# Optimization experiments

Hardware: AMD Instinct MI355X
Metric: run time of the kernel (lower is better)

Reference implementation:

```python
import jax, jax.numpy as jnp
import numpy as np

H, NH, NKV, HD, FF = 2048, 16, 8, 128, 6144
S, T = 2048, 4096
EPS, THETA, NEG = 1e-6, 1e6, -1e9

def _rms(x, w, eps=EPS):
    return x * jax.lax.rsqrt(jnp.mean(x * x, axis=-1, keepdims=True) + eps) * w

def _rotate_half(x):
    d = x.shape[-1] // 2
    return jnp.concatenate([-x[..., d:], x[..., :d]], axis=-1)

def _rope(positions, hd, theta=THETA):
    inv_freq = 1.0 / (theta ** (jnp.arange(0, hd, 2, dtype=jnp.float32) / hd))
    freqs = positions.astype(jnp.float32)[..., None] * inv_freq  # [B,S,hd/2]
    emb = jnp.concatenate([freqs, freqs], axis=-1)               # [B,S,hd]
    return jnp.cos(emb), jnp.sin(emb)

def setup_inputs() -> dict:
    key = jax.random.key(0)
    ks = jax.random.split(key, 12)
    hidden_states = jax.random.normal(ks[0], (1, S, H), jnp.float32) * 0.02
    i = jnp.arange(T)
    causal_mask = jnp.where(i[None, :] <= i[:, None], 0.0, NEG).astype(jnp.float32)[None, None]
    idxs = jnp.sort(jax.random.randint(ks[1], (S,), 0, T - 1, jnp.int32)).at[-1].set(T - 1)
    w = lambda k, sh: jax.random.normal(k, sh, jnp.float32) * 0.02
    return dict(
        hidden_states=hidden_states, causal_mask=causal_mask,
        keys_idxs=idxs, hs_idxs=idxs, positions=idxs[None, :],
        ln_in_w=jnp.ones((H,), jnp.float32),
        q_w=w(ks[2], (H, NH * HD)), k_w=w(ks[3], (H, NKV * HD)), v_w=w(ks[4], (H, NKV * HD)),
        q_norm_w=jnp.ones((HD,), jnp.float32), k_norm_w=jnp.ones((HD,), jnp.float32),
        o_w=w(ks[5], (NH * HD, H)), ln_post_w=jnp.ones((H,), jnp.float32),
        gate_w=w(ks[6], (H, FF)), up_w=w(ks[7], (H, FF)), down_w=w(ks[8], (FF, H)),
    )

def reference(hidden_states, causal_mask, keys_idxs, hs_idxs, positions,
              ln_in_w, q_w, k_w, v_w, q_norm_w, k_norm_w, o_w,
              ln_post_w, gate_w, up_w, down_w):
    B, Sq, _ = hidden_states.shape
    hd = q_norm_w.shape[0]
    nh = q_w.shape[1] // hd
    nkv = k_w.shape[1] // hd
    scaling = hd ** -0.5

    # gather pruned causal mask: index_select dim 3 (keys), then dim 2 (queries)
    mask = causal_mask[:, :, :, keys_idxs][:, :, hs_idxs, :]  # [B,1,Sq,Sk]

    cos, sin = _rope(positions, hd)  # [B,Sq,hd]

    x = _rms(hidden_states, ln_in_w)
    q = _rms((x @ q_w).reshape(B, Sq, nh, hd), q_norm_w).swapaxes(1, 2)   # [B,nh,Sq,hd]
    k = _rms((x @ k_w).reshape(B, Sq, nkv, hd), k_norm_w).swapaxes(1, 2)  # [B,nkv,Sq,hd]
    v = (x @ v_w).reshape(B, Sq, nkv, hd).swapaxes(1, 2)

    c, s = cos[:, None], sin[:, None]
    q = q * c + _rotate_half(q) * s
    k = k * c + _rotate_half(k) * s

    groups = nh // nkv
    k_rep = jnp.repeat(k, groups, axis=1)
    v_rep = jnp.repeat(v, groups, axis=1)

    # token-importance from last query (last original token kept at slot Sq-1)
    q_last = q[:, :, -1:, :]
    imp = jax.nn.softmax(jnp.einsum('bhqd,bhkd->bhqk', q_last, k_rep) * scaling, axis=-1)
    importance = imp[0, :, 0, :].mean(axis=0)
    importance = jax.lax.stop_gradient(importance.at[Sq - 1].set(jnp.inf))

    scores = jnp.einsum('bhqd,bhkd->bhqk', q, k_rep) * scaling + mask
    attn = jax.nn.softmax(scores, axis=-1)
    ctx = jnp.einsum('bhqk,bhkd->bhqd', attn, v_rep)
    attn_out = ctx.swapaxes(1, 2).reshape(B, Sq, nh * hd) @ o_w

    h = hidden_states + attn_out
    y = _rms(h, ln_post_w)
    mlp = (jax.nn.silu(y @ gate_w) * (y @ up_w)) @ down_w
    out = h + mlp
    return out, importance
```

## Files before the change

### kernel.cpp

```cpp
#include <hip/hip_runtime.h>
#include <math.h>

#define S_LEN 2048
#define HDIM  2048
#define NHEADS 16
#define NKVH   8
#define HD     128
#define FFDIM  6144
#define EPSV   1e-6f

__device__ __forceinline__ ushort f2bf(float f) {
    unsigned u = __float_as_uint(f);
    u += 0x7FFF + ((u >> 16) & 1);
    return (ushort)(u >> 16);
}
__device__ __forceinline__ float bf2f(ushort h) {
    return __uint_as_float(((unsigned)h) << 16);
}

typedef __attribute__((ext_vector_type(8))) short bf16x8;
typedef __attribute__((ext_vector_type(4))) float f32x4;

__device__ __forceinline__ void glds16(const void* g, void* l) {
    __builtin_amdgcn_global_load_lds(
// ... 17 lines not shown
    red[tid] = ss;
    __syncthreads();
    for (int off = 128; off > 0; off >>= 1) {
        if (tid < off) red[tid] += red[tid + off];
        __syncthreads();
    }
    float r = rsqrtf(red[0] / (float)HDIM + EPSV);
    for (int i = tid; i < HDIM; i += 256) {
        float v = row[i] * r * w[i];
        ushort h = f2bf(v);
        oh[(size_t)s * HDIM + i] = h;
        ol[(size_t)s * HDIM + i] = f2bf(v - bf2f(h));
    }
}

__global__ __launch_bounds__(256) void conv_q_k(const float* __restrict__ in,
                                                ushort* __restrict__ oh,
                                                ushort* __restrict__ ol) {
    int i = blockIdx.x * 256 + threadIdx.x;
    int s = i >> 11, c = i & 2047;
    float v = in[(size_t)s * 4096 + c];
    ushort h = f2bf(v);
    oh[i] = h;
    ol[i] = f2bf(v - bf2f(h));
}

__global__ __launch_bounds__(256) void conv_k_swz_k(const float* __restrict__ in,
                                                    ushort* __restrict__ oh,
                                                    ushort* __restrict__ ol) {
    int i = blockIdx.x * 256 + threadIdx.x;
    int s = i >> 10, c = i & 1023;
    int d = c & 127;
    float v = in[(size_t)s * 4096 + 2048 + c];
    unsigned u = __float_as_uint(v);
    float hi = __uint_as_float(u & 0xFFFF0000u);
    int o = (i & ~127) + (d ^ ((s & 7) << 3));
    oh[o] = (ushort)(u >> 16);
    ol[o] = (ushort)(__float_as_uint(v - hi) >> 16);
}

__global__ __launch_bounds__(256) void conv_vt_k(const float* __restrict__ vsrc,
                                                 ushort* __restrict__ oh,
                                                 ushort* __restrict__ ol) {
    __shared__ float t[64][65];
    int s0 = blockIdx.x * 64, d0 = blockIdx.y * 64, kvh = blockIdx.z;
    int tid = threadIdx.x;
#pragma unroll
    for (int p = 0; p < 4; ++p) {
        int c = tid + p * 256;
        int ss = c >> 4, d4 = (c & 15) * 4;
        float4 x = *(const float4*)&vsrc[(size_t)(s0 + ss) * 4096 + 3072 + kvh * 128 + d0 + d4];
        t[d4 + 0][ss] = x.x;
        t[d4 + 1][ss] = x.y;
// ... 9 lines not shown
        int sx = s4 ^ ((d & 7) << 3);
        size_t obase = ((size_t)kvh * HD + d) * S_LEN + s0 + sx;
        ushort4 hv, lv;
        float a0 = t[dd][s4 + 0], a1 = t[dd][s4 + 1], a2 = t[dd][s4 + 2], a3 = t[dd][s4 + 3];
        unsigned u0 = __float_as_uint(a0), u1 = __float_as_uint(a1);
        unsigned u2 = __float_as_uint(a2), u3 = __float_as_uint(a3);
        hv.x = (ushort)(u0 >> 16); lv.x = (ushort)(__float_as_uint(a0 - __uint_as_float(u0 & 0xFFFF0000u)) >> 16);
        hv.y = (ushort)(u1 >> 16); lv.y = (ushort)(__float_as_uint(a1 - __uint_as_float(u1 & 0xFFFF0000u)) >> 16);
        hv.z = (ushort)(u2 >> 16); lv.z = (ushort)(__float_as_uint(a2 - __uint_as_float(u2 & 0xFFFF0000u)) >> 16);
        hv.w = (ushort)(u3 >> 16); lv.w = (ushort)(__float_as_uint(a3 - __uint_as_float(u3 & 0xFFFF0000u)) >> 16);
        *(ushort4*)&oh[obase] = hv;
        *(ushort4*)&ol[obase] = lv;
    }
}

__global__ __launch_bounds__(256) void transpose_split_k(const float* __restrict__ W,
                                                         ushort* __restrict__ Th,
                                                         ushort* __restrict__ Tl,
                                                         int K, int Ntot, int n0,
                                                         int nout0) {
    __shared__ float t[64][65];
    int tid = threadIdx.x;
    int nt = blockIdx.x * 64;
    int kt = blockIdx.y * 64;
#pragma unroll
    for (int p = 0; p < 4; ++p) {
        int idx = tid + p * 256;
        int kk = idx >> 4;
        int nn = (idx & 15) * 4;
        float4 v = *(const float4*)&W[(size_t)(kt + kk) * Ntot + n0 + nt + nn];
        t[nn + 0][kk] = v.x;
        t[nn + 1][kk] = v.y;
        t[nn + 2][kk] = v.z;
        t[nn + 3][kk] = v.w;
    }
    __syncthreads();
#pragma unroll
    for (int p = 0; p < 4; ++p) {
        int idx = tid + p * 256;
        int nn = idx >> 4;
        int kk = (idx & 15) * 4;
        ushort4 hv, lv;
        float a0 = t[nn][kk + 0], a1 = t[nn][kk + 1], a2 = t[nn][kk + 2], a3 = t[nn][kk + 3];
        hv.x = f2bf(a0); lv.x = f2bf(a0 - bf2f(hv.x));
        hv.y = f2bf(a1); lv.y = f2bf(a1 - bf2f(hv.y));
        hv.z = f2bf(a2); lv.z = f2bf(a2 - bf2f(hv.z));
        hv.w = f2bf(a3); lv.w = f2bf(a3 - bf2f(hv.w));
        size_t o = (size_t)(nout0 + nt + nn) * K + kt + kk;
        *(ushort4*)&Th[o] = hv;
        *(ushort4*)&Tl[o] = lv;
    }
}

__global__ __launch_bounds__(256, 2) void gemm_bf16x3(
    const ushort* __restrict__ Ah, const ushort* __restrict__ Al,
    const ushort* __restrict__ Bh, const ushort* __restrict__ Bl,
    const float* __restrict__ res, float* __restrict__ C,
    int M, int N, int K) {
    __shared__ __align__(16) ushort sAh[2][128 * 32];
    __shared__ __align__(16) ushort sAl[2][128 * 32];
    __shared__ __align__(16) ushort sBh[2][128 * 32];
    __shared__ __align__(16) ushort sBl[2][128 * 32];

    unsigned nbx = gridDim.x;
    unsigned flat = blockIdx.y * nbx + blockIdx.x;
    unsigned cpx = (nbx * gridDim.y) >> 3;
    unsigned sflat = (flat & 7u) * cpx + (flat >> 3);
    int bx = (int)(sflat % nbx);
    int by = (int)(sflat / nbx);
    int bm = by * 128, bn = bx * 128;

    int tid = threadIdx.x;
// ... 44 lines not shown
            }
        }
    };

    STAGE(0, 0);
    __syncthreads();
    int cur = 0;
    for (int k0 = 32; k0 < K; k0 += 32) {
        STAGE(cur ^ 1, k0);
        COMPUTE(cur);
        __syncthreads();
        cur ^= 1;
    }
    COMPUTE(cur);

    int c0 = bn + wc * 64 + r;
    int r0 = bm + wr * 64 + kq * 4;
#pragma unroll
    for (int mi = 0; mi < 4; ++mi)
#pragma unroll
        for (int ni = 0; ni < 4; ++ni)
#pragma unroll
            for (int j = 0; j < 4; ++j) {
                int row = r0 + mi * 16 + j;
                int col = c0 + ni * 16;
                size_t idx = (size_t)row * N + col;
                float val = acc[mi][ni][j];
                if (res) val += res[idx];
                C[idx] = val;
            }
}

__global__ __launch_bounds__(128) void qk_norm_rope_k(float* __restrict__ qk,
                                                      const float* __restrict__ nw,
                                                      const int* __restrict__ positions,
                                                      int stride) {
    int s = blockIdx.x;
    int h = blockIdx.y;
    int d = threadIdx.x;
    float* row = qk + (size_t)s * stride + (size_t)h * HD;
    __shared__ float buf[HD];
    __shared__ float red[HD];
    float v = row[d];
    red[d] = v * v;
    __syncthreads();
    for (int off = 64; off > 0; off >>= 1) {
        if (d < off) red[d] += red[d + off];
        __syncthreads();
    }
    float r = rsqrtf(red[0] / (float)HD + EPSV);
    float nv = v * r * nw[d];
    buf[d] = nv;
    __syncthreads();
    float pos = (float)positions[s];
    int d2 = d & 63;
    float inv_freq = expf(-((float)(2 * d2) / 128.0f) * 13.815510557964274f);
    float freq = pos * inv_freq;
    float c, sn;
    sincosf(freq, &sn, &c);
    float rot = (d < 64) ? -buf[d + 64] : buf[d - 64];
    row[d] = nv * c + rot * sn;
}

#define ATQ 64
#define ATK 64

__global__ __launch_bounds__(256, 2) void attn_mfma_k(
    const ushort* __restrict__ Qhg, const ushort* __restrict__ Qlg,
    const ushort* __restrict__ Khg, const ushort* __restrict__ Klg,
    const ushort* __restrict__ Vhg, const ushort* __restrict__ Vlg,
    const int* __restrict__ keys_idxs, const int* __restrict__ hs_idxs,
    ushort* __restrict__ Chg, ushort* __restrict__ Clg) {
    __shared__ __align__(16) ushort sKh[64 * 128];
    __shared__ __align__(16) ushort sKl[64 * 128];
    __shared__ __align__(16) ushort sVh[128 * 64];
    __shared__ __align__(16) ushort sVl[128 * 64];
    __shared__ int kidx[ATK];
    __shared__ int qpos[ATQ];

    int bx = blockIdx.x;
    int qt = (bx & 1) ? (31 - (bx >> 1)) : (bx >> 1);
    int h = blockIdx.y;
    int kvh = h >> 1;
    int tid = threadIdx.x;
    int lane = tid & 63, wv = tid >> 6;
    int q0 = qt * ATQ;
    int r = lane & 15, kq = lane >> 4;
    int xorv = (lane & 7) << 3;
    const float scale = 0.088388347648318447f;

    bf16x8 qh[4], ql[4];
    {
        const ushort* qb = Qhg + ((size_t)(q0 + wv * 16 + r) * NHEADS + h) * HD + kq * 8;
        const ushort* qb2 = Qlg + ((size_t)(q0 + wv * 16 + r) * NHEADS + h) * HD + kq * 8;
#pragma unroll
        for (int ks = 0; ks < 4; ++ks) {
            qh[ks] = *(const bf16x8*)(qb + ks * 32);
            ql[ks] = *(const bf16x8*)(qb2 + ks * 32);
        }
    }
    if (tid < ATQ) qpos[tid] = hs_idxs[q0 + tid];

    const size_t kvstride = (size_t)NKVH * HD;
    const ushort* gKh = Khg + ((size_t)(tid >> 4) * NKVH + kvh) * HD + (tid & 15) * 8;
    const ushort* gKl = Klg + ((size_t)(tid >> 4) * NKVH + kvh) * HD + (tid & 15) * 8;
    const ushort* gVh = Vhg + ((size_t)kvh * HD + (tid >> 3)) * S_LEN + (tid & 7) * 8;
    const ushort* gVl = Vlg + ((size_t)kvh * HD + (tid >> 3)) * S_LEN + (tid & 7) * 8;

    f32x4 o[8] = {};
    float m_run[4] = {-3.0e38f, -3.0e38f, -3.0e38f, -3.0e38f};
    float l_run[4] = {0.0f, 0.0f, 0.0f, 0.0f};

    __syncthreads();
    int hs_max = qpos[ATQ - 1];
    int qp[4];
#pragma unroll
    for (int j = 0; j < 4; ++j) qp[j] = qpos[wv * 16 + kq * 4 + j];

    for (int kt = 0; kt < S_LEN / ATK; ++kt) {
        int k0 = kt * ATK;
        if (keys_idxs[k0] > hs_max) break;
        __syncthreads();
        const size_t koff = (size_t)k0 * kvstride;
#pragma unroll
        for (int p = 0; p < 4; ++p) {
            glds16(gKh + koff + (size_t)p * 16 * kvstride, sKh + (tid + p * 256) * 8);
            glds16(gKl + koff + (size_t)p * 16 * kvstride, sKl + (tid + p * 256) * 8);
            glds16(gVh + k0 + (size_t)p * 32 * S_LEN, sVh + (tid + p * 256) * 8);
            glds16(gVl + k0 + (size_t)p * 32 * S_LEN, sVl + (tid + p * 256) * 8);
        }
        if (tid < ATK) kidx[tid] = keys_idxs[k0 + tid];
        __syncthreads();

        f32x4 sf[4] = {};
#pragma unroll
        for (int ks = 0; ks < 4; ++ks) {
            int kb = (ks * 32 + kq * 8) ^ xorv;
#pragma unroll
            for (int f = 0; f < 4; ++f) {
                bf16x8 kh = *(const bf16x8*)(sKh + (f * 16 + r) * 128 + kb);
                bf16x8 kl = *(const bf16x8*)(sKl + (f * 16 + r) * 128 + kb);
                sf[f] = __builtin_amdgcn_mfma_f32_16x16x32_bf16(qh[ks], kh, sf[f], 0, 0, 0);
                sf[f] = __builtin_amdgcn_mfma_f32_16x16x32_bf16(ql[ks], kh, sf[f], 0, 0, 0);
                sf[f] = __builtin_amdgcn_mfma_f32_16x16x32_bf16(qh[ks], kl, sf[f], 0, 0, 0);
            }
        }

        int kj[4];
#pragma unroll
        for (int f = 0; f < 4; ++f) kj[f] = kidx[f * 16 + r];
        float alj[4];
#pragma unroll
        for (int j = 0; j < 4; ++j) {
#pragma unroll
            for (int f = 0; f < 4; ++f)
                sf[f][j] = sf[f][j] * scale + ((kj[f] <= qp[j]) ? 0.0f : -1.0e9f);
            float m0 = fmaxf(fmaxf(sf[0][j], sf[1][j]), fmaxf(sf[2][j], sf[3][j]));
#pragma unroll
            for (int off = 1; off < 16; off <<= 1) m0 = fmaxf(m0, __shfl_xor(m0, off));
            float mn = fmaxf(m_run[j], m0);
            alj[j] = __expf(m_run[j] - mn);
            m_run[j] = mn;
            float rsum = 0.0f;
#pragma unroll
            for (int f = 0; f < 4; ++f) {
                sf[f][j] = __expf(sf[f][j] - mn);
                rsum += sf[f][j];
            }
#pragma unroll
            for (int off = 1; off < 16; off <<= 1) rsum += __shfl_xor(rsum, off);
            l_run[j] = l_run[j] * alj[j] + rsum;
        }
#pragma unroll
        for (int df = 0; df < 8; ++df)
#pragma unroll
            for (int j = 0; j < 4; ++j) o[df][j] *= alj[j];

        __syncthreads();

        ushort* sPh = sKh + wv * 2048;
        ushort* sPl = sPh + 1024;
#pragma unroll
        for (int j = 0; j < 4; ++j) {
            int qloc = kq * 4 + j;
            int swz = (qloc & 7) << 3;
            int rowb = qloc * 64;
#pragma unroll
            for (int f = 0; f < 4; ++f) {
                float pv = sf[f][j];
                unsigned u = __float_as_uint(pv);
                float hi = __uint_as_float(u & 0xFFFF0000u);
                int a = rowb + ((f * 16 + r) ^ swz);
                sPh[a] = (ushort)(u >> 16);
                sPl[a] = (ushort)(__float_as_uint(pv - hi) >> 16);
            }
        }

#pragma unroll
        for (int kv0 = 0; kv0 < 2; ++kv0) {
            int kb = (kv0 * 32 + kq * 8) ^ xorv;
            bf16x8 pah = *(const bf16x8*)(sPh + r * 64 + kb);
            bf16x8 pal = *(const bf16x8*)(sPl + r * 64 + kb);
#pragma unroll
            for (int df = 0; df < 8; ++df) {
                bf16x8 vh = *(const bf16x8*)(sVh + (df * 16 + r) * 64 + kb);
                bf16x8 vl = *(const bf16x8*)(sVl + (df * 16 + r) * 64 + kb);
                o[df] = __builtin_amdgcn_mfma_f32_16x16x32_bf16(pah, vh, o[df], 0, 0, 0);
                o[df] = __builtin_amdgcn_mfma_f32_16x16x32_bf16(pal, vh, o[df], 0, 0, 0);
                o[df] = __builtin_amdgcn_mfma_f32_16x16x32_bf16(pah, vl, o[df], 0, 0, 0);
            }
        }
    }

#pragma unroll
    for (int j = 0; j < 4; ++j) {
        float invl = 1.0f / l_run[j];
        int qg = q0 + wv * 16 + kq * 4 + j;
#pragma unroll
        for (int df = 0; df < 8; ++df) {
            int d = df * 16 + r;
            float val = o[df][j] * invl;
            size_t idx = ((size_t)qg * NHEADS + h) * HD + d;
            ushort hh = f2bf(val);
            Chg[idx] = hh;
            Clg[idx] = f2bf(val - bf2f(hh));
        }
    }
}

__global__ __launch_bounds__(256) void importance_scores_k(const float* __restrict__ q,
                                                           const float* __restrict__ k,
                                                           float* __restrict__ imp_ws,
                                                           int stride) {
    int h = blockIdx.x;
    int kv = h >> 1;
    int tid = threadIdx.x;
    __shared__ float qrow[HD];
    __shared__ float sc[S_LEN];
    __shared__ float red[256];
    const float* qp = q + (size_t)(S_LEN - 1) * stride + (size_t)h * HD;
    if (tid < HD) qrow[tid] = qp[tid];
    __syncthreads();
    const float scale = 0.088388347648318447f;
    float lmax = -3.0e38f;
#pragma unroll
    for (int rep = 0; rep < 8; ++rep) {
        int j = tid + rep * 256;
        const float* kp = k + (size_t)j * stride + (size_t)kv * HD;
        float dot = 0.0f;
        for (int d = 0; d < HD; ++d) dot += qrow[d] * kp[d];
        float sval = dot * scale;
        sc[j] = sval;
        lmax = fmaxf(lmax, sval);
    }
    red[tid] = lmax;
    __syncthreads();
    for (int off = 128; off > 0; off >>= 1) {
        if (tid < off) red[tid] = fmaxf(red[tid], red[tid + off]);
        __syncthreads();
    }
    float m = red[0];
    __syncthreads();
    float lsum = 0.0f;
    float evals[8];
#pragma unroll
// ... 11 lines not shown
    }
    float inv = 1.0f / red[0];
#pragma unroll
    for (int rep = 0; rep < 8; ++rep) {
        int j = tid + rep * 256;
        imp_ws[(size_t)h * S_LEN + j] = evals[rep] * inv;
    }
}

__global__ __launch_bounds__(256) void importance_combine_k(const float* __restrict__ imp_ws,
                                                            float* __restrict__ out) {
    int j = blockIdx.x * 256 + threadIdx.x;
    float sum = 0.0f;
    for (int h = 0; h < NHEADS; ++h) sum += imp_ws[(size_t)h * S_LEN + j];
    out[j] = (j == S_LEN - 1) ? 3.0e38f : sum * (1.0f / NHEADS);
}

__global__ __launch_bounds__(256) void silu_split_k(const float* __restrict__ gu,
                                                    ushort* __restrict__ dh,
                                                    ushort* __restrict__ dl) {
    int i = blockIdx.x * 256 + threadIdx.x;
    int s = i >> 11, c = i & 2047;
    const float* row = gu + (size_t)s * 4096;
    float g = row[c], u = row[c + 2048];
    float d = g / (1.0f + expf(-g)) * u;
    ushort hh = f2bf(d);
    dh[i] = hh;
    dl[i] = f2bf(d - bf2f(hh));
}

extern "C" void kernel_launch(void* const* d_in, const int* in_sizes, int n_in,
                              void* d_out, int out_size, void* d_ws, size_t ws_size,
                              hipStream_t stream) {
    const float* hidden    = (const float*)d_in[0];
    const int*   keys_idxs = (const int*)d_in[2];
    const int*   hs_idxs   = (const int*)d_in[3];
    const int*   positions = (const int*)d_in[4];
    const float* ln_in_w   = (const float*)d_in[5];
    const float* q_w       = (const float*)d_in[6];
    const float* k_w       = (const float*)d_in[7];
    const float* v_w       = (const float*)d_in[8];
    const float* q_norm_w  = (const float*)d_in[9];
    const float* k_norm_w  = (const float*)d_in[10];
// ... 7 lines not shown
    float* ws = (float*)d_ws;
    const size_t MF = 1024ull * 1024;

    ushort* Xh  = (ushort*)(ws);
    ushort* Xl  = (ushort*)(ws + 2 * MF);
    ushort* Wh  = (ushort*)(ws + 4 * MF);
    ushort* Wl  = (ushort*)(ws + 8 * MF);
    float*  qkv = ws + 12 * MF;
    ushort* Qbh = (ushort*)(ws);
    ushort* Qbl = (ushort*)(ws + 2 * MF);
    ushort* Kbh = (ushort*)(ws + 4 * MF);
    ushort* Kbl = (ushort*)(ws + 5 * MF);
    ushort* Vth = (ushort*)(ws + 6 * MF);
    ushort* Vtl = (ushort*)(ws + 7 * MF);
    float*  imp = ws + 8 * MF;
    ushort* Woh = (ushort*)(ws + 4 * MF);
    ushort* Wol = (ushort*)(ws + 6 * MF);
    ushort* Ch  = (ushort*)(ws + 12 * MF);
    ushort* Cl  = (ushort*)(ws + 14 * MF);
    float*  hb  = ws + 16 * MF;
    ushort* Yh  = (ushort*)(ws);
    ushort* Yl  = (ushort*)(ws + 2 * MF);
    float*  gu  = ws + 12 * MF;
    ushort* Dh  = (ushort*)(ws + 4 * MF);
    ushort* Dl  = (ushort*)(ws + 6 * MF);
    ushort* Wdh = (ushort*)(ws + 8 * MF);
    ushort* Wdl = (ushort*)(ws + 10 * MF);

    rmsnorm_split_k<<<S_LEN, 256, 0, stream>>>(hidden, ln_in_w, Xh, Xl);

    transpose_split_k<<<dim3(32, 32), 256, 0, stream>>>(q_w, Wh, Wl, HDIM, HDIM, 0, 0);
    transpose_split_k<<<dim3(16, 32), 256, 0, stream>>>(k_w, Wh, Wl, HDIM, 1024, 0, 2048);
    transpose_split_k<<<dim3(16, 32), 256, 0, stream>>>(v_w, Wh, Wl, HDIM, 1024, 0, 3072);
    gemm_bf16x3<<<dim3(4096 / 128, S_LEN / 128), 256, 0, stream>>>(
        Xh, Xl, Wh, Wl, nullptr, qkv, S_LEN, 4096, HDIM);

    qk_norm_rope_k<<<dim3(S_LEN, NHEADS), 128, 0, stream>>>(qkv, q_norm_w, positions, 4096);
    qk_norm_rope_k<<<dim3(S_LEN, NKVH), 128, 0, stream>>>(qkv + 2048, k_norm_w, positions, 4096);

    importance_scores_k<<<NHEADS, 256, 0, stream>>>(qkv, qkv + 2048, imp, 4096);
    importance_combine_k<<<S_LEN / 256, 256, 0, stream>>>(imp, out + (size_t)S_LEN * HDIM);

    conv_q_k<<<(S_LEN * 2048) / 256, 256, 0, stream>>>(qkv, Qbh, Qbl);
    conv_k_swz_k<<<(S_LEN * 1024) / 256, 256, 0, stream>>>(qkv, Kbh, Kbl);
    conv_vt_k<<<dim3(S_LEN / 64, HD / 64, NKVH), 256, 0, stream>>>(qkv, Vth, Vtl);

    attn_mfma_k<<<dim3(S_LEN / ATQ, NHEADS), 256, 0, stream>>>(
        Qbh, Qbl, Kbh, Kbl, Vth, Vtl, keys_idxs, hs_idxs, Ch, Cl);

    transpose_split_k<<<dim3(32, 32), 256, 0, stream>>>(o_w, Woh, Wol, HDIM, HDIM, 0, 0);
    gemm_bf16x3<<<dim3(HDIM / 128, S_LEN / 128), 256, 0, stream>>>(
        Ch, Cl, Woh, Wol, hidden, hb, S_LEN, HDIM, HDIM);

    hipMemcpyAsync(out, hb, (size_t)S_LEN * HDIM * sizeof(float),
                   hipMemcpyDeviceToDevice, stream);

    rmsnorm_split_k<<<S_LEN, 256, 0, stream>>>(hb, ln_post_w, Yh, Yl);

    for (int c = 0; c < 3; ++c) {
        transpose_split_k<<<dim3(32, 32), 256, 0, stream>>>(gate_w, Wh, Wl, HDIM, FFDIM, c * 2048, 0);
        transpose_split_k<<<dim3(32, 32), 256, 0, stream>>>(up_w, Wh, Wl, HDIM, FFDIM, c * 2048, 2048);
        gemm_bf16x3<<<dim3(4096 / 128, S_LEN / 128), 256, 0, stream>>>(
            Yh, Yl, Wh, Wl, nullptr, gu, S_LEN, 4096, HDIM);
        silu_split_k<<<(S_LEN * 2048) / 256, 256, 0, stream>>>(gu, Dh, Dl);
        transpose_split_k<<<dim3(32, 32), 256, 0, stream>>>(
            down_w + (size_t)c * 2048 * HDIM, Wdh, Wdl, 2048, HDIM, 0, 0);
        gemm_bf16x3<<<dim3(HDIM / 128, S_LEN / 128), 256, 0, stream>>>(
            Dh, Dl, Wdh, Wdl, out, out, S_LEN, HDIM, 2048);
    }
}
```

Baseline: 1.362 ms.

## Fuse QK-norm/RoPE with bf16 split, SiLU into GEMM epilogue, restructure attention

Several changes land together. QK RMSNorm and RoPE now write the hi/lo bf16 split directly, which removes the separate conversion kernels, and importance scoring reads those split buffers. Gate/up weights are interleaved per 64 columns so the gate/up GEMM can apply SiLU*up in its epilogue through LDS, which drops the gu buffer and the silu kernel. The attention kernel uses 128-query tiles with double-buffered K/V and pairs a front tile with a back tile per block to balance causal work. The q/k/v weight transposes are merged into one launch, and the residual copy is folded into the o-proj GEMM epilogue.

Result: slower. 1.591 ms (+16.9%).

```diff
diff --git a/kernel.cpp b/kernel.cpp
--- a/kernel.cpp
+++ b/kernel.cpp
@@ -55,29 +55,124 @@
     }
 }
 
-__global__ __launch_bounds__(256) void conv_q_k(const float* __restrict__ in,
-                                                ushort* __restrict__ oh,
-                                                ushort* __restrict__ ol) {
-    int i = blockIdx.x * 256 + threadIdx.x;
-    int s = i >> 11, c = i & 2047;
-    float v = in[(size_t)s * 4096 + c];
-    ushort h = f2bf(v);
-    oh[i] = h;
-    ol[i] = f2bf(v - bf2f(h));
-}
-
-__global__ __launch_bounds__(256) void conv_k_swz_k(const float* __restrict__ in,
-                                                    ushort* __restrict__ oh,
-                                                    ushort* __restrict__ ol) {
-    int i = blockIdx.x * 256 + threadIdx.x;
-    int s = i >> 10, c = i & 1023;
-    int d = c & 127;
-    float v = in[(size_t)s * 4096 + 2048 + c];
-    unsigned u = __float_as_uint(v);
-    float hi = __uint_as_float(u & 0xFFFF0000u);
-    int o = (i & ~127) + (d ^ ((s & 7) << 3));
-    oh[o] = (ushort)(u >> 16);
-    ol[o] = (ushort)(__float_as_uint(v - hi) >> 16);
+__global__ __launch_bounds__(256) void transpose_split_qkv_k(
+    const float* __restrict__ q_w, const float* __restrict__ k_w,
+    const float* __restrict__ v_w, ushort* __restrict__ Th,
+    ushort* __restrict__ Tl) {
+    int z = blockIdx.z;
+    int bx = blockIdx.x;
+    if (z > 0 && bx >= 16) return;
+    const float* W = (z == 0) ? q_w : ((z == 1) ? k_w : v_w);
+    int Ntot = (z == 0) ? 2048 : 1024;
+    int nout0 = (z == 0) ? 0 : ((z == 1) ? 2048 : 3072);
+    __shared__ float t[64][65];
+    int tid = threadIdx.x;
+    int nt = bx * 64;
+    int kt = blockIdx.y * 64;
+#pragma unroll
+    for (int p = 0; p < 4; ++p) {
+        int idx = tid + p * 256;
+        int kk = idx >> 4;
+        int nn = (idx & 15) * 4;
+        float4 v = *(const float4*)&W[(size_t)(kt + kk) * Ntot + nt + nn];
+        t[nn + 0][kk] = v.x;
+        t[nn + 1][kk] = v.y;
+        t[nn + 2][kk] = v.z;
+        t[nn + 3][kk] = v.w;
+    }
+    __syncthreads();
+#pragma unroll
+    for (int p = 0; p < 4; ++p) {
+        int idx = tid + p * 256;
+        int nn = idx >> 4;
+        int kk = (idx & 15) * 4;
+        ushort4 hv, lv;
+        float a0 = t[nn][kk + 0], a1 = t[nn][kk + 1], a2 = t[nn][kk + 2], a3 = t[nn][kk + 3];
+        hv.x = f2bf(a0); lv.x = f2bf(a0 - bf2f(hv.x));
+        hv.y = f2bf(a1); lv.y = f2bf(a1 - bf2f(hv.y));
+        hv.z = f2bf(a2); lv.z = f2bf(a2 - bf2f(hv.z));
+        hv.w = f2bf(a3); lv.w = f2bf(a3 - bf2f(hv.w));
+        size_t o = (size_t)(nout0 + nt + nn) * HDIM + kt + kk;
+        *(ushort4*)&Th[o] = hv;
+        *(ushort4*)&Tl[o] = lv;
+    }
+}
+
+__global__ __launch_bounds__(256) void transpose_split_k(const float* __restrict__ W,
+                                                         ushort* __restrict__ Th,
+                                                         ushort* __restrict__ Tl,
+                                                         int K, int Ntot, int n0,
+                                                         int nout0) {
+    __shared__ float t[64][65];
+    int tid = threadIdx.x;
+    int nt = blockIdx.x * 64;
+    int kt = blockIdx.y * 64;
+#pragma unroll
+    for (int p = 0; p < 4; ++p) {
+        int idx = tid + p * 256;
+        int kk = idx >> 4;
+        int nn = (idx & 15) * 4;
+        float4 v = *(const float4*)&W[(size_t)(kt + kk) * Ntot + n0 + nt + nn];
+        t[nn + 0][kk] = v.x;
+        t[nn + 1][kk] = v.y;
+        t[nn + 2][kk] = v.z;
+        t[nn + 3][kk] = v.w;
+    }
+    __syncthreads();
+#pragma unroll
+    for (int p = 0; p < 4; ++p) {
+        int idx = tid + p * 256;
+        int nn = idx >> 4;
+        int kk = (idx & 15) * 4;
+        ushort4 hv, lv;
+        float a0 = t[nn][kk + 0], a1 = t[nn][kk + 1], a2 = t[nn][kk + 2], a3 = t[nn][kk + 3];
+        hv.x = f2bf(a0); lv.x = f2bf(a0 - bf2f(hv.x));
+        hv.y = f2bf(a1); lv.y = f2bf(a1 - bf2f(hv.y));
+        hv.z = f2bf(a2); lv.z = f2bf(a2 - bf2f(hv.z));
+        hv.w = f2bf(a3); lv.w = f2bf(a3 - bf2f(hv.w));
+        size_t o = (size_t)(nout0 + nt + nn) * K + kt + kk;
+        *(ushort4*)&Th[o] = hv;
+        *(ushort4*)&Tl[o] = lv;
+    }
+}
+
+__global__ __launch_bounds__(256) void transpose_split_gu_k(
+    const float* __restrict__ gate_w, const float* __restrict__ up_w,
+    ushort* __restrict__ Th, ushort* __restrict__ Tl, int n0) {
+    int z = blockIdx.z;
+    const float* W = z ? up_w : gate_w;
+    __shared__ float t[64][65];
+    int tid = threadIdx.x;
+    int bx = blockIdx.x;
+    int kt = blockIdx.y * 64;
+    int nout0 = 128 * bx + 64 * z;
+#pragma unroll
+    for (int p = 0; p < 4; ++p) {
+        int idx = tid + p * 256;
+        int kk = idx >> 4;
+        int nn = (idx & 15) * 4;
+        float4 v = *(const float4*)&W[(size_t)(kt + kk) * FFDIM + n0 + bx * 64 + nn];
+        t[nn + 0][kk] = v.x;
+        t[nn + 1][kk] = v.y;
+        t[nn + 2][kk] = v.z;
+        t[nn + 3][kk] = v.w;
+    }
+    __syncthreads();
+#pragma unroll
+    for (int p = 0; p < 4; ++p) {
+        int idx = tid + p * 256;
+        int nn = idx >> 4;
+        int kk = (idx & 15) * 4;
+        ushort4 hv, lv;
+        float a0 = t[nn][kk + 0], a1 = t[nn][kk + 1], a2 = t[nn][kk + 2], a3 = t[nn][kk + 3];
+        hv.x = f2bf(a0); lv.x = f2bf(a0 - bf2f(hv.x));
+        hv.y = f2bf(a1); lv.y = f2bf(a1 - bf2f(hv.y));
+        hv.z = f2bf(a2); lv.z = f2bf(a2 - bf2f(hv.z));
+        hv.w = f2bf(a3); lv.w = f2bf(a3 - bf2f(hv.w));
+        size_t o = (size_t)(nout0 + nn) * HDIM + kt + kk;
+        *(ushort4*)&Th[o] = hv;
+        *(ushort4*)&Tl[o] = lv;
+    }
 }
 
 __global__ __launch_bounds__(256) void conv_vt_k(const float* __restrict__ vsrc,
@@ -117,48 +212,48 @@
     }
 }
 
-__global__ __launch_bounds__(256) void transpose_split_k(const float* __restrict__ W,
-                                                         ushort* __restrict__ Th,
-                                                         ushort* __restrict__ Tl,
-                                                         int K, int Ntot, int n0,
-                                                         int nout0) {
-    __shared__ float t[64][65];
-    int tid = threadIdx.x;
-    int nt = blockIdx.x * 64;
-    int kt = blockIdx.y * 64;
-#pragma unroll
-    for (int p = 0; p < 4; ++p) {
-        int idx = tid + p * 256;
-        int kk = idx >> 4;
-        int nn = (idx & 15) * 4;
-        float4 v = *(const float4*)&W[(size_t)(kt + kk) * Ntot + n0 + nt + nn];
-        t[nn + 0][kk] = v.x;
-        t[nn + 1][kk] = v.y;
-        t[nn + 2][kk] = v.z;
-        t[nn + 3][kk] = v.w;
-    }
-    __syncthreads();
-#pragma unroll
-    for (int p = 0; p < 4; ++p) {
-        int idx = tid + p * 256;
-        int nn = idx >> 4;
-        int kk = (idx & 15) * 4;
-        ushort4 hv, lv;
-        float a0 = t[nn][kk + 0], a1 = t[nn][kk + 1], a2 = t[nn][kk + 2], a3 = t[nn][kk + 3];
-        hv.x = f2bf(a0); lv.x = f2bf(a0 - bf2f(hv.x));
-        hv.y = f2bf(a1); lv.y = f2bf(a1 - bf2f(hv.y));
-        hv.z = f2bf(a2); lv.z = f2bf(a2 - bf2f(hv.z));
-        hv.w = f2bf(a3); lv.w = f2bf(a3 - bf2f(hv.w));
-        size_t o = (size_t)(nout0 + nt + nn) * K + kt + kk;
-        *(ushort4*)&Th[o] = hv;
-        *(ushort4*)&Tl[o] = lv;
-    }
-}
-
+__global__ __launch_bounds__(128) void qk_rope_split_k(
+    const float* __restrict__ qkv, const float* __restrict__ nw,
+    const int* __restrict__ positions, ushort* __restrict__ oh,
+    ushort* __restrict__ ol, int nheads, int coloff, int swz) {
+    int s = blockIdx.x;
+    int h = blockIdx.y;
+    int d = threadIdx.x;
+    const float* row = qkv + (size_t)s * 4096 + coloff + h * HD;
+    __shared__ float buf[HD];
+    __shared__ float red[HD];
+    float v = row[d];
+    red[d] = v * v;
+    __syncthreads();
+    for (int off = 64; off > 0; off >>= 1) {
+        if (d < off) red[d] += red[d + off];
+        __syncthreads();
+    }
+    float r = rsqrtf(red[0] / (float)HD + EPSV);
+    float nv = v * r * nw[d];
+    buf[d] = nv;
+    __syncthreads();
+    float pos = (float)positions[s];
+    int d2 = d & 63;
+    float inv_freq = expf(-((float)(2 * d2) / 128.0f) * 13.815510557964274f);
+    float freq = pos * inv_freq;
+    float c, sn;
+    sincosf(freq, &sn, &c);
+    float rot = (d < 64) ? -buf[d + 64] : buf[d - 64];
+    float val = nv * c + rot * sn;
+    int dd = swz ? (d ^ ((s & 7) << 3)) : d;
+    size_t o = ((size_t)s * nheads + h) * HD + dd;
+    ushort hh = f2bf(val);
+    oh[o] = hh;
+    ol[o] = f2bf(val - bf2f(hh));
+}
+
+template <int MODE>
 __global__ __launch_bounds__(256, 2) void gemm_bf16x3(
     const ushort* __restrict__ Ah, const ushort* __restrict__ Al,
     const ushort* __restrict__ Bh, const ushort* __restrict__ Bl,
     const float* __restrict__ res, float* __restrict__ C,
+    float* __restrict__ C2, ushort* __restrict__ Dh, ushort* __restrict__ Dl,
     int M, int N, int K) {
     __shared__ __align__(16) ushort sAh[2][128 * 32];
     __shared__ __align__(16) ushort sAl[2][128 * 32];
@@ -233,6 +328,41 @@
     }
     COMPUTE(cur);
 
+    if (MODE == 2) {
+        __syncthreads();
+        float* X = (wr == 0) ? (float*)sAh : (float*)sBh;
+        if (wc == 1) {
+#pragma unroll
+            for (int mi = 0; mi < 4; ++mi)
+#pragma unroll
+                for (int ni = 0; ni < 4; ++ni)
+#pragma unroll
+                    for (int j = 0; j < 4; ++j)
+                        X[(mi * 16 + kq * 4 + j) * 64 + ni * 16 + r] = acc[mi][ni][j];
+        }
+        __syncthreads();
+        if (wc == 0) {
+            int ND = N >> 1;
+#pragma unroll
+            for (int mi = 0; mi < 4; ++mi)
+#pragma unroll
+                for (int ni = 0; ni < 4; ++ni)
+#pragma unroll
+                    for (int j = 0; j < 4; ++j) {
+                        float g = acc[mi][ni][j];
+                        float u = X[(mi * 16 + kq * 4 + j) * 64 + ni * 16 + r];
+                        float dv = g / (1.0f + expf(-g)) * u;
+                        int row = bm + wr * 64 + kq * 4 + mi * 16 + j;
+                        int col = (bn >> 1) + ni * 16 + r;
+                        size_t idx = (size_t)row * ND + col;
+                        ushort hh = f2bf(dv);
+                        Dh[idx] = hh;
+                        Dl[idx] = f2bf(dv - bf2f(hh));
+                    }
+        }
+        return;
+    }
+
     int c0 = bn + wc * 64 + r;
     int r0 = bm + wr * 64 + kq * 4;
 #pragma unroll
@@ -247,227 +377,241 @@
                 float val = acc[mi][ni][j];
                 if (res) val += res[idx];
                 C[idx] = val;
+                if (MODE == 1) C2[idx] = val;
             }
 }
 
-__global__ __launch_bounds__(128) void qk_norm_rope_k(float* __restrict__ qk,
-                                                      const float* __restrict__ nw,
-                                                      const int* __restrict__ positions,
-                                                      int stride) {
-    int s = blockIdx.x;
-    int h = blockIdx.y;
-    int d = threadIdx.x;
-    float* row = qk + (size_t)s * stride + (size_t)h * HD;
-    __shared__ float buf[HD];
-    __shared__ float red[HD];
-    float v = row[d];
-    red[d] = v * v;
-    __syncthreads();
-    for (int off = 64; off > 0; off >>= 1) {
-        if (d < off) red[d] += red[d + off];
-        __syncthreads();
-    }
-    float r = rsqrtf(red[0] / (float)HD + EPSV);
-    float nv = v * r * nw[d];
-    buf[d] = nv;
-    __syncthreads();
-    float pos = (float)positions[s];
-    int d2 = d & 63;
-    float inv_freq = expf(-((float)(2 * d2) / 128.0f) * 13.815510557964274f);
-    float freq = pos * inv_freq;
-    float c, sn;
-    sincosf(freq, &sn, &c);
-    float rot = (d < 64) ? -buf[d + 64] : buf[d - 64];
-    row[d] = nv * c + rot * sn;
-}
-
-#define ATQ 64
 #define ATK 64
 
-__global__ __launch_bounds__(256, 2) void attn_mfma_k(
+__global__ __launch_bounds__(256, 1) void attn_mfma_k(
     const ushort* __restrict__ Qhg, const ushort* __restrict__ Qlg,
     const ushort* __restrict__ Khg, const ushort* __restrict__ Klg,
     const ushort* __restrict__ Vhg, const ushort* __restrict__ Vlg,
     const int* __restrict__ keys_idxs, const int* __restrict__ hs_idxs,
     ushort* __restrict__ Chg, ushort* __restrict__ Clg) {
-    __shared__ __align__(16) ushort sKh[64 * 128];
-    __shared__ __align__(16) ushort sKl[64 * 128];
-    __shared__ __align__(16) ushort sVh[128 * 64];
-    __shared__ __align__(16) ushort sVl[128 * 64];
-    __shared__ int kidx[ATK];
-    __shared__ int qpos[ATQ];
-
-    int bx = blockIdx.x;
-    int qt = (bx & 1) ? (31 - (bx >> 1)) : (bx >> 1);
+    __shared__ __align__(16) ushort sKh[2][64 * 128];
+    __shared__ __align__(16) ushort sKl[2][64 * 128];
+    __shared__ __align__(16) ushort sVh[2][128 * 64];
+    __shared__ __align__(16) ushort sVl[2][128 * 64];
+    __shared__ int kidx[2][ATK];
+    __shared__ int qpos[128];
+
     int h = blockIdx.y;
     int kvh = h >> 1;
     int tid = threadIdx.x;
     int lane = tid & 63, wv = tid >> 6;
-    int q0 = qt * ATQ;
     int r = lane & 15, kq = lane >> 4;
     int xorv = (lane & 7) << 3;
     const float scale = 0.088388347648318447f;
-
-    bf16x8 qh[4], ql[4];
-    {
-        const ushort* qb = Qhg + ((size_t)(q0 + wv * 16 + r) * NHEADS + h) * HD + kq * 8;
-        const ushort* qb2 = Qlg + ((size_t)(q0 + wv * 16 + r) * NHEADS + h) * HD + kq * 8;
-#pragma unroll
-        for (int ks = 0; ks < 4; ++ks) {
-            qh[ks] = *(const bf16x8*)(qb + ks * 32);
-            ql[ks] = *(const bf16x8*)(qb2 + ks * 32);
-        }
-    }
-    if (tid < ATQ) qpos[tid] = hs_idxs[q0 + tid];
-
     const size_t kvstride = (size_t)NKVH * HD;
+
     const ushort* gKh = Khg + ((size_t)(tid >> 4) * NKVH + kvh) * HD + (tid & 15) * 8;
     const ushort* gKl = Klg + ((size_t)(tid >> 4) * NKVH + kvh) * HD + (tid & 15) * 8;
     const ushort* gVh = Vhg + ((size_t)kvh * HD + (tid >> 3)) * S_LEN + (tid & 7) * 8;
     const ushort* gVl = Vlg + ((size_t)kvh * HD + (tid >> 3)) * S_LEN + (tid & 7) * 8;
 
-    f32x4 o[8] = {};
-    float m_run[4] = {-3.0e38f, -3.0e38f, -3.0e38f, -3.0e38f};
-    float l_run[4] = {0.0f, 0.0f, 0.0f, 0.0f};
-
-    __syncthreads();
-    int hs_max = qpos[ATQ - 1];
-    int qp[4];
-#pragma unroll
-    for (int j = 0; j < 4; ++j) qp[j] = qpos[wv * 16 + kq * 4 + j];
-
-    for (int kt = 0; kt < S_LEN / ATK; ++kt) {
-        int k0 = kt * ATK;
-        if (keys_idxs[k0] > hs_max) break;
-        __syncthreads();
-        const size_t koff = (size_t)k0 * kvstride;
-#pragma unroll
-        for (int p = 0; p < 4; ++p) {
-            glds16(gKh + koff + (size_t)p * 16 * kvstride, sKh + (tid + p * 256) * 8);
-            glds16(gKl + koff + (size_t)p * 16 * kvstride, sKl + (tid + p * 256) * 8);
-            glds16(gVh + k0 + (size_t)p * 32 * S_LEN, sVh + (tid + p * 256) * 8);
-            glds16(gVl + k0 + (size_t)p * 32 * S_LEN, sVl + (tid + p * 256) * 8);
-        }
-        if (tid < ATK) kidx[tid] = keys_idxs[k0 + tid];
-        __syncthreads();
-
-        f32x4 sf[4] = {};
-#pragma unroll
-        for (int ks = 0; ks < 4; ++ks) {
-            int kb = (ks * 32 + kq * 8) ^ xorv;
-#pragma unroll
-            for (int f = 0; f < 4; ++f) {
-                bf16x8 kh = *(const bf16x8*)(sKh + (f * 16 + r) * 128 + kb);
-                bf16x8 kl = *(const bf16x8*)(sKl + (f * 16 + r) * 128 + kb);
-                sf[f] = __builtin_amdgcn_mfma_f32_16x16x32_bf16(qh[ks], kh, sf[f], 0, 0, 0);
-                sf[f] = __builtin_amdgcn_mfma_f32_16x16x32_bf16(ql[ks], kh, sf[f], 0, 0, 0);
-                sf[f] = __builtin_amdgcn_mfma_f32_16x16x32_bf16(qh[ks], kl, sf[f], 0, 0, 0);
+    for (int sub = 0; sub < 2; ++sub) {
+        int qt = (sub == 0) ? blockIdx.x : (15 - blockIdx.x);
+        int q0 = qt * 128;
+        if (tid < 128) qpos[tid] = hs_idxs[q0 + tid];
+
+        bf16x8 qh[2][4], ql[2][4];
+#pragma unroll
+        for (int fr = 0; fr < 2; ++fr) {
+            int qrow = q0 + wv * 32 + fr * 16 + r;
+            const ushort* qb = Qhg + ((size_t)qrow * NHEADS + h) * HD + kq * 8;
+            const ushort* qb2 = Qlg + ((size_t)qrow * NHEADS + h) * HD + kq * 8;
+#pragma unroll
+            for (int ks = 0; ks < 4; ++ks) {
+                qh[fr][ks] = *(const bf16x8*)(qb + ks * 32);
+                ql[fr][ks] = *(const bf16x8*)(qb2 + ks * 32);
             }
         }
 
-        int kj[4];
-#pragma unroll
-        for (int f = 0; f < 4; ++f) kj[f] = kidx[f * 16 + r];
-        float alj[4];
-#pragma unroll
-        for (int j = 0; j < 4; ++j) {
-#pragma unroll
-            for (int f = 0; f < 4; ++f)
-                sf[f][j] = sf[f][j] * scale + ((kj[f] <= qp[j]) ? 0.0f : -1.0e9f);
-            float m0 = fmaxf(fmaxf(sf[0][j], sf[1][j]), fmaxf(sf[2][j], sf[3][j]));
-#pragma unroll
-            for (int off = 1; off < 16; off <<= 1) m0 = fmaxf(m0, __shfl_xor(m0, off));
-            float mn = fmaxf(m_run[j], m0);
-            alj[j] = __expf(m_run[j] - mn);
-            m_run[j] = mn;
-            float rsum = 0.0f;
-#pragma unroll
-            for (int f = 0; f < 4; ++f) {
-                sf[f][j] = __expf(sf[f][j] - mn);
-                rsum += sf[f][j];
+#pragma unroll
+        for (int p = 0; p < 4; ++p) {
+            glds16(gKh + (size_t)p * 16 * kvstride, &sKh[0][(tid + p * 256) * 8]);
+            glds16(gKl + (size_t)p * 16 * kvstride, &sKl[0][(tid + p * 256) * 8]);
+            glds16(gVh + (size_t)p * 32 * S_LEN, &sVh[0][(tid + p * 256) * 8]);
+            glds16(gVl + (size_t)p * 32 * S_LEN, &sVl[0][(tid + p * 256) * 8]);
+        }
+        if (tid < ATK) kidx[0][tid] = keys_idxs[tid];
+        __syncthreads();
+
+        int hs_max = qpos[127];
+        int qp[2][4];
+#pragma unroll
+        for (int fr = 0; fr < 2; ++fr)
+#pragma unroll
+            for (int j = 0; j < 4; ++j) qp[fr][j] = qpos[wv * 32 + fr * 16 + kq * 4 + j];
+
+        f32x4 o[2][8] = {};
+        float m_run[2][4] = {{-3.0e38f, -3.0e38f, -3.0e38f, -3.0e38f},
+                             {-3.0e38f, -3.0e38f, -3.0e38f, -3.0e38f}};
+        float l_run[2][4] = {};
+        int cur = 0;
+
+        for (int kt = 0;; ++kt) {
+            int k0 = kt * ATK;
+            if (k0 >= S_LEN || keys_idxs[k0] > hs_max) break;
+            int kn = (k0 + ATK < S_LEN) ? (k0 + ATK) : k0;
+            {
+                int nb = cur ^ 1;
+                const size_t koff = (size_t)kn * kvstride;
+#pragma unroll
+                for (int p = 0; p < 4; ++p) {
+                    glds16(gKh + koff + (size_t)p * 16 * kvstride, &sKh[nb][(tid + p * 256) * 8]);
+                    glds16(gKl + koff + (size_t)p * 16 * kvstride, &sKl[nb][(tid + p * 256) * 8]);
+                    glds16(gVh + kn + (size_t)p * 32 * S_LEN, &sVh[nb][(tid + p * 256) * 8]);
+                    glds16(gVl + kn + (size_t)p * 32 * S_LEN, &sVl[nb][(tid + p * 256) * 8]);
+                }
+                if (tid < ATK) kidx[nb][tid] = keys_idxs[kn + tid];
             }
-#pragma unroll
-            for (int off = 1; off < 16; off <<= 1) rsum += __shfl_xor(rsum, off);
-            l_run[j] = l_run[j] * alj[j] + rsum;
+
+            f32x4 sf[2][4] = {};
+#pragma unroll
+            for (int ks = 0; ks < 4; ++ks) {
+                int kb = (ks * 32 + kq * 8) ^ xorv;
+#pragma unroll
+                for (int f = 0; f < 4; ++f) {
+                    bf16x8 kh = *(const bf16x8*)(&sKh[cur][(f * 16 + r) * 128 + kb]);
+                    bf16x8 kl = *(const bf16x8*)(&sKl[cur][(f * 16 + r) * 128 + kb]);
+#pragma unroll
+                    for (int fr = 0; fr < 2; ++fr) {
+                        sf[fr][f] = __builtin_amdgcn_mfma_f32_16x16x32_bf16(qh[fr][ks], kh, sf[fr][f], 0, 0, 0);
+                        sf[fr][f] = __builtin_amdgcn_mfma_f32_16x16x32_bf16(ql[fr][ks], kh, sf[fr][f], 0, 0, 0);
+                        sf[fr][f] = __builtin_amdgcn_mfma_f32_16x16x32_bf16(qh[fr][ks], kl, sf[fr][f], 0, 0, 0);
+                    }
+                }
+            }
+
+            int kj[4];
+#pragma unroll
+            for (int f = 0; f < 4; ++f) kj[f] = kidx[cur][f * 16 + r];
+            float alj[2][4];
+#pragma unroll
+            for (int fr = 0; fr < 2; ++fr)
+#pragma unroll
+                for (int j = 0; j < 4; ++j) {
+#pragma unroll
+                    for (int f = 0; f < 4; ++f)
+                        sf[fr][f][j] = sf[fr][f][j] * scale + ((kj[f] <= qp[fr][j]) ? 0.0f : -1.0e9f);
+                    float m0 = fmaxf(fmaxf(sf[fr][0][j], sf[fr][1][j]), fmaxf(sf[fr][2][j], sf[fr][3][j]));
+#pragma unroll
+                    for (int off = 1; off < 16; off <<= 1) m0 = fmaxf(m0, __shfl_xor(m0, off));
+                    float mn = fmaxf(m_run[fr][j], m0);
+                    alj[fr][j] = __expf(m_run[fr][j] - mn);
+                    m_run[fr][j] = mn;
+                    float rsum = 0.0f;
+#pragma unroll
+                    for (int f = 0; f < 4; ++f) {
+                        sf[fr][f][j] = __expf(sf[fr][f][j] - mn);
+                        rsum += sf[fr][f][j];
+                    }
+#pragma unroll
+                    for (int off = 1; off < 16; off <<= 1) rsum += __shfl_xor(rsum, off);
+                    l_run[fr][j] = l_run[fr][j] * alj[fr][j] + rsum;
+                }
+#pragma unroll
+            for (int fr = 0; fr < 2; ++fr)
+#pragma unroll
+                for (int df = 0; df < 8; ++df)
+#pragma unroll
+                    for (int j = 0; j < 4; ++j) o[fr][df][j] *= alj[fr][j];
+
+            __syncthreads();
+
+#pragma unroll
+            for (int fr = 0; fr < 2; ++fr)
+#pragma unroll
+                for (int j = 0; j < 4; ++j) {
+                    int qloc = wv * 32 + fr * 16 + kq * 4 + j;
+                    int swz = (qloc & 7) << 3;
+                    int rowb = qloc * 64;
+#pragma unroll
+                    for (int f = 0; f < 4; ++f) {
+                        float pv = sf[fr][f][j];
+                        unsigned u = __float_as_uint(pv);
+                        float hi = __uint_as_float(u & 0xFFFF0000u);
+                        int a = rowb + ((f * 16 + r) ^ swz);
+                        sKh[cur][a] = (ushort)(u >> 16);
+                        sKl[cur][a] = (ushort)(__float_as_uint(pv - hi) >> 16);
+                    }
+                }
+
+#pragma unroll
+            for (int kv0 = 0; kv0 < 2; ++kv0) {
+                int kb = (kv0 * 32 + kq * 8) ^ xorv;
+                bf16x8 pah[2], pal[2];
+#pragma unroll
+                for (int fr = 0; fr < 2; ++fr) {
+                    int prow = wv * 32 + fr * 16 + r;
+                    pah[fr] = *(const bf16x8*)(&sKh[cur][prow * 64 + kb]);
+                    pal[fr] = *(const bf16x8*)(&sKl[cur][prow * 64 + kb]);
+                }
+#pragma unroll
+                for (int df = 0; df < 8; ++df) {
+                    bf16x8 vh = *(const bf16x8*)(&sVh[cur][(df * 16 + r) * 64 + kb]);
+                    bf16x8 vl = *(const bf16x8*)(&sVl[cur][(df * 16 + r) * 64 + kb]);
+#pragma unroll
+                    for (int fr = 0; fr < 2; ++fr) {
+                        o[fr][df] = __builtin_amdgcn_mfma_f32_16x16x32_bf16(pah[fr], vh, o[fr][df], 0, 0, 0);
+                        o[fr][df] = __builtin_amdgcn_mfma_f32_16x16x32_bf16(pal[fr], vh, o[fr][df], 0, 0, 0);
+                        o[fr][df] = __builtin_amdgcn_mfma_f32_16x16x32_bf16(pah[fr], vl, o[fr][df], 0, 0, 0);
+                    }
+                }
+            }
+            __syncthreads();
+            cur ^= 1;
         }
-#pragma unroll
-        for (int df = 0; df < 8; ++df)
-#pragma unroll
-            for (int j = 0; j < 4; ++j) o[df][j] *= alj[j];
-
-        __syncthreads();
-
-        ushort* sPh = sKh + wv * 2048;
-        ushort* sPl = sPh + 1024;
-#pragma unroll
-        for (int j = 0; j < 4; ++j) {
-            int qloc = kq * 4 + j;
-            int swz = (qloc & 7) << 3;
-            int rowb = qloc * 64;
-#pragma unroll
-            for (int f = 0; f < 4; ++f) {
-                float pv = sf[f][j];
-                unsigned u = __float_as_uint(pv);
-                float hi = __uint_as_float(u & 0xFFFF0000u);
-                int a = rowb + ((f * 16 + r) ^ swz);
-                sPh[a] = (ushort)(u >> 16);
-                sPl[a] = (ushort)(__float_as_uint(pv - hi) >> 16);
+
+#pragma unroll
+        for (int fr = 0; fr < 2; ++fr)
+#pragma unroll
+            for (int j = 0; j < 4; ++j) {
+                float invl = 1.0f / l_run[fr][j];
+                int qg = q0 + wv * 32 + fr * 16 + kq * 4 + j;
+#pragma unroll
+                for (int df = 0; df < 8; ++df) {
+                    int d = df * 16 + r;
+                    float val = o[fr][df][j] * invl;
+                    size_t idx = ((size_t)qg * NHEADS + h) * HD + d;
+                    ushort hh = f2bf(val);
+                    Chg[idx] = hh;
+                    Clg[idx] = f2bf(val - bf2f(hh));
+                }
             }
-        }
-
-#pragma unroll
-        for (int kv0 = 0; kv0 < 2; ++kv0) {
-            int kb = (kv0 * 32 + kq * 8) ^ xorv;
-            bf16x8 pah = *(const bf16x8*)(sPh + r * 64 + kb);
-            bf16x8 pal = *(const bf16x8*)(sPl + r * 64 + kb);
-#pragma unroll
-            for (int df = 0; df < 8; ++df) {
-                bf16x8 vh = *(const bf16x8*)(sVh + (df * 16 + r) * 64 + kb);
-                bf16x8 vl = *(const bf16x8*)(sVl + (df * 16 + r) * 64 + kb);
-                o[df] = __builtin_amdgcn_mfma_f32_16x16x32_bf16(pah, vh, o[df], 0, 0, 0);
-                o[df] = __builtin_amdgcn_mfma_f32_16x16x32_bf16(pal, vh, o[df], 0, 0, 0);
-                o[df] = __builtin_amdgcn_mfma_f32_16x16x32_bf16(pah, vl, o[df], 0, 0, 0);
-            }
-        }
-    }
-
-#pragma unroll
-    for (int j = 0; j < 4; ++j) {
-        float invl = 1.0f / l_run[j];
-        int qg = q0 + wv * 16 + kq * 4 + j;
-#pragma unroll
-        for (int df = 0; df < 8; ++df) {
-            int d = df * 16 + r;
-            float val = o[df][j] * invl;
-            size_t idx = ((size_t)qg * NHEADS + h) * HD + d;
-            ushort hh = f2bf(val);
-            Chg[idx] = hh;
-            Clg[idx] = f2bf(val - bf2f(hh));
-        }
-    }
-}
-
-__global__ __launch_bounds__(256) void importance_scores_k(const float* __restrict__ q,
-                                                           const float* __restrict__ k,
-                                                           float* __restrict__ imp_ws,
-                                                           int stride) {
+        __syncthreads();
+    }
+}
+
+__global__ __launch_bounds__(256) void importance_scores_k(
+    const ushort* __restrict__ Qh, const ushort* __restrict__ Ql,
+    const ushort* __restrict__ Kh, const ushort* __restrict__ Kl,
+    float* __restrict__ imp_ws) {
     int h = blockIdx.x;
     int kv = h >> 1;
     int tid = threadIdx.x;
     __shared__ float qrow[HD];
     __shared__ float sc[S_LEN];
     __shared__ float red[256];
-    const float* qp = q + (size_t)(S_LEN - 1) * stride + (size_t)h * HD;
-    if (tid < HD) qrow[tid] = qp[tid];
+    if (tid < HD) {
+        size_t qi = ((size_t)(S_LEN - 1) * NHEADS + h) * HD + tid;
+        qrow[tid] = bf2f(Qh[qi]) + bf2f(Ql[qi]);
+    }
     __syncthreads();
     const float scale = 0.088388347648318447f;
     float lmax = -3.0e38f;
 #pragma unroll
     for (int rep = 0; rep < 8; ++rep) {
         int j = tid + rep * 256;
-        const float* kp = k + (size_t)j * stride + (size_t)kv * HD;
+        size_t base = ((size_t)j * NKVH + kv) * HD;
+        int swz = (j & 7) << 3;
         float dot = 0.0f;
-        for (int d = 0; d < HD; ++d) dot += qrow[d] * kp[d];
+        for (int d = 0; d < HD; ++d) {
+            int dd = d ^ swz;
+            dot += qrow[d] * (bf2f(Kh[base + dd]) + bf2f(Kl[base + dd]));
+        }
         float sval = dot * scale;
         sc[j] = sval;
         lmax = fmaxf(lmax, sval);
@@ -509,19 +653,6 @@
     float sum = 0.0f;
     for (int h = 0; h < NHEADS; ++h) sum += imp_ws[(size_t)h * S_LEN + j];
     out[j] = (j == S_LEN - 1) ? 3.0e38f : sum * (1.0f / NHEADS);
-}
-
-__global__ __launch_bounds__(256) void silu_split_k(const float* __restrict__ gu,
-                                                    ushort* __restrict__ dh,
-                                                    ushort* __restrict__ dl) {
-    int i = blockIdx.x * 256 + threadIdx.x;
-    int s = i >> 11, c = i & 2047;
-    const float* row = gu + (size_t)s * 4096;
-    float g = row[c], u = row[c + 2048];
-    float d = g / (1.0f + expf(-g)) * u;
-    ushort hh = f2bf(d);
-    dh[i] = hh;
-    dl[i] = f2bf(d - bf2f(hh));
 }
 
 extern "C" void kernel_launch(void* const* d_in, const int* in_sizes, int n_in,
@@ -559,58 +690,50 @@
     ushort* Vth = (ushort*)(ws + 6 * MF);
     ushort* Vtl = (ushort*)(ws + 7 * MF);
     float*  imp = ws + 8 * MF;
-    ushort* Woh = (ushort*)(ws + 4 * MF);
-    ushort* Wol = (ushort*)(ws + 6 * MF);
-    ushort* Ch  = (ushort*)(ws + 12 * MF);
-    ushort* Cl  = (ushort*)(ws + 14 * MF);
-    float*  hb  = ws + 16 * MF;
+    ushort* Ch  = (ushort*)(ws + 8 * MF);
+    ushort* Cl  = (ushort*)(ws + 10 * MF);
+    float*  hb  = ws + 12 * MF;
+    ushort* Woh = (ushort*)(ws + 16 * MF);
+    ushort* Wol = (ushort*)(ws + 18 * MF);
     ushort* Yh  = (ushort*)(ws);
     ushort* Yl  = (ushort*)(ws + 2 * MF);
-    float*  gu  = ws + 12 * MF;
-    ushort* Dh  = (ushort*)(ws + 4 * MF);
-    ushort* Dl  = (ushort*)(ws + 6 * MF);
-    ushort* Wdh = (ushort*)(ws + 8 * MF);
-    ushort* Wdl = (ushort*)(ws + 10 * MF);
+    ushort* Dh  = (ushort*)(ws + 12 * MF);
+    ushort* Dl  = (ushort*)(ws + 14 * MF);
+    ushort* Wdh = (ushort*)(ws + 16 * MF);
+    ushort* Wdl = (ushort*)(ws + 18 * MF);
 
     rmsnorm_split_k<<<S_LEN, 256, 0, stream>>>(hidden, ln_in_w, Xh, Xl);
 
-    transpose_split_k<<<dim3(32, 32), 256, 0, stream>>>(q_w, Wh, Wl, HDIM, HDIM, 0, 0);
-    transpose_split_k<<<dim3(16, 32), 256, 0, stream>>>(k_w, Wh, Wl, HDIM, 1024, 0, 2048);
-    transpose_split_k<<<dim3(16, 32), 256, 0, stream>>>(v_w, Wh, Wl, HDIM, 1024, 0, 3072);
-    gemm_bf16x3<<<dim3(4096 / 128, S_LEN / 128), 256, 0, stream>>>(
-        Xh, Xl, Wh, Wl, nullptr, qkv, S_LEN, 4096, HDIM);
-
-    qk_norm_rope_k<<<dim3(S_LEN, NHEADS), 128, 0, stream>>>(qkv, q_norm_w, positions, 4096);
-    qk_norm_rope_k<<<dim3(S_LEN, NKVH), 128, 0, stream>>>(qkv + 2048, k_norm_w, positions, 4096);
-
-    importance_scores_k<<<NHEADS, 256, 0, stream>>>(qkv, qkv + 2048, imp, 4096);
+    transpose_split_qkv_k<<<dim3(32, 32, 3), 256, 0, stream>>>(q_w, k_w, v_w, Wh, Wl);
+    gemm_bf16x3<0><<<dim3(32, 16), 256, 0, stream>>>(
+        Xh, Xl, Wh, Wl, nullptr, qkv, nullptr, nullptr, nullptr, S_LEN, 4096, HDIM);
+
+    qk_rope_split_k<<<dim3(S_LEN, NHEADS), 128, 0, stream>>>(
+        qkv, q_norm_w, positions, Qbh, Qbl, NHEADS, 0, 0);
+    qk_rope_split_k<<<dim3(S_LEN, NKVH), 128, 0, stream>>>(
+        qkv, k_norm_w, positions, Kbh, Kbl, NKVH, 2048, 1);
+
+    conv_vt_k<<<dim3(S_LEN / 64, HD / 64, NKVH), 256, 0, stream>>>(qkv, Vth, Vtl);
+
+    importance_scores_k<<<NHEADS, 256, 0, stream>>>(Qbh, Qbl, Kbh, Kbl, imp);
     importance_combine_k<<<S_LEN / 256, 256, 0, stream>>>(imp, out + (size_t)S_LEN * HDIM);
 
-    conv_q_k<<<(S_LEN * 2048) / 256, 256, 0, stream>>>(qkv, Qbh, Qbl);
-    conv_k_swz_k<<<(S_LEN * 1024) / 256, 256, 0, stream>>>(qkv, Kbh, Kbl);
-    conv_vt_k<<<dim3(S_LEN / 64, HD / 64, NKVH), 256, 0, stream>>>(qkv, Vth, Vtl);
-
-    attn_mfma_k<<<dim3(S_LEN / ATQ, NHEADS), 256, 0, stream>>>(
+    attn_mfma_k<<<dim3(16, 16), 256, 0, stream>>>(
         Qbh, Qbl, Kbh, Kbl, Vth, Vtl, keys_idxs, hs_idxs, Ch, Cl);
 
     transpose_split_k<<<dim3(32, 32), 256, 0, stream>>>(o_w, Woh, Wol, HDIM, HDIM, 0, 0);
-    gemm_bf16x3<<<dim3(HDIM / 128, S_LEN / 128), 256, 0, stream>>>(
-        Ch, Cl, Woh, Wol, hidden, hb, S_LEN, HDIM, HDIM);
-
-    hipMemcpyAsync(out, hb, (size_t)S_LEN * HDIM * sizeof(float),
-                   hipMemcpyDeviceToDevice, stream);
+    gemm_bf16x3<1><<<dim3(16, 16), 256, 0, stream>>>(
+        Ch, Cl, Woh, Wol, hidden, hb, out, nullptr, nullptr, S_LEN, HDIM, HDIM);
 
     rmsnorm_split_k<<<S_LEN, 256, 0, stream>>>(hb, ln_post_w, Yh, Yl);
 
     for (int c = 0; c < 3; ++c) {
-        transpose_split_k<<<dim3(32, 32), 256, 0, stream>>>(gate_w, Wh, Wl, HDIM, FFDIM, c * 2048, 0);
-        transpose_split_k<<<dim3(32, 32), 256, 0, stream>>>(up_w, Wh, Wl, HDIM, FFDIM, c * 2048, 2048);
-        gemm_bf16x3<<<dim3(4096 / 128, S_LEN / 128), 256, 0, stream>>>(
-            Yh, Yl, Wh, Wl, nullptr, gu, S_LEN, 4096, HDIM);
-        silu_split_k<<<(S_LEN * 2048) / 256, 256, 0, stream>>>(gu, Dh, Dl);
+        transpose_split_gu_k<<<dim3(32, 32, 2), 256, 0, stream>>>(gate_w, up_w, Wh, Wl, c * 2048);
+        gemm_bf16x3<2><<<dim3(32, 16), 256, 0, stream>>>(
+            Yh, Yl, Wh, Wl, nullptr, nullptr, nullptr, Dh, Dl, S_LEN, 4096, HDIM);
         transpose_split_k<<<dim3(32, 32), 256, 0, stream>>>(
             down_w + (size_t)c * 2048 * HDIM, Wdh, Wdl, 2048, HDIM, 0, 0);
-        gemm_bf16x3<<<dim3(HDIM / 128, S_LEN / 128), 256, 0, stream>>>(
-            Dh, Dl, Wdh, Wdl, out, out, S_LEN, HDIM, 2048);
-    }
-}
+        gemm_bf16x3<0><<<dim3(16, 16), 256, 0, stream>>>(
+            Dh, Dl, Wdh, Wdl, out, out, nullptr, nullptr, nullptr, S_LEN, HDIM, 2048);
+    }
+}
```
